# Performance work log

Measured on AMD Instinct MI355X. Metric: run time of the kernel, lower is better.

Reference implementation:

```python
import jax, jax.numpy as jnp
import numpy as np

N_NODES = 100000
IN_F = 256
OUT_F = 256
N_EDGES = 3200000


def setup_inputs() -> dict:
    key = jax.random.key(0)
    ks = jax.random.split(key, 10)
    return {
        "mean": jax.random.normal(ks[0], (N_NODES, IN_F), dtype=jnp.float32),
        "var": jax.random.uniform(ks[1], (N_NODES, IN_F), dtype=jnp.float32),
        "W_mean": jax.random.normal(ks[2], (IN_F, OUT_F), dtype=jnp.float32) * (1.0 / np.sqrt(IN_F)),
        "b_mean": jax.random.normal(ks[3], (OUT_F,), dtype=jnp.float32) * 0.01,
        "W_var": jax.random.normal(ks[4], (IN_F, OUT_F), dtype=jnp.float32) * (1.0 / np.sqrt(IN_F)),
        "b_var": jax.random.normal(ks[5], (OUT_F,), dtype=jnp.float32) * 0.01,
        "edge_row": jax.random.randint(ks[6], (N_EDGES,), 0, N_NODES, dtype=jnp.int32),
        "edge_col": jax.random.randint(ks[7], (N_EDGES,), 0, N_NODES, dtype=jnp.int32),
        "adj0_vals": jax.random.uniform(ks[8], (N_EDGES,), dtype=jnp.float32),
        "adj1_vals": jax.random.uniform(ks[9], (N_EDGES,), dtype=jnp.float32),
    }


def _spmm(row, col, vals, x, n_nodes):
    # out[i] = sum_{e: row[e]==i} vals[e] * x[col[e]]
    gathered = x[col] * vals[:, None]  # [E, F]
    return jax.ops.segment_sum(gathered, row, num_segments=n_nodes)


def reference(mean, var, W_mean, b_mean, W_var, b_var, edge_row, edge_col, adj0_vals, adj1_vals):
    m = jnp.dot(mean, W_mean) + b_mean          # mean_conv
    v = jnp.dot(var, W_var) + b_var             # var_conv (initial=False)
    m = jax.nn.elu(m)                           # act0
    v = jax.nn.relu(v)                          # act1
    attention = jnp.exp(-v)
    m = m * attention
    v = v * attention * attention
    m = _spmm(edge_row, edge_col, adj0_vals, m, mean.shape[0])
    v = _spmm(edge_row, edge_col, adj1_vals, v, mean.shape[0])
    return (m, v)
```

## Files before the change

kernel.cpp:

```cpp
#include <hip/hip_runtime.h>
#include <hip/hip_bf16.h>
#include <stdint.h>

#define F 256
#define KSTEP 32

typedef short bhalf8 __attribute__((ext_vector_type(8)));
typedef unsigned short ushort8v __attribute__((ext_vector_type(8)));
typedef float f32x4 __attribute__((ext_vector_type(4)));
typedef int i32x4 __attribute__((ext_vector_type(4)));

__device__ __forceinline__ unsigned short f2b(float f) {
    union { float f; uint32_t u; } x; x.f = f;
    uint32_t u = x.u;
    return (unsigned short)((u + 0x7FFFu + ((u >> 16) & 1u)) >> 16);
}
__device__ __forceinline__ float b2f(unsigned short h) {
    union { uint32_t u; float f; } x; x.u = ((uint32_t)h) << 16;
    return x.f;
}

__global__ __launch_bounds__(256) void setup_kernel(
    const float* __restrict__ Wm, const float* __restrict__ Wv,
    unsigned short* __restrict__ Wt, int* __restrict__ count, int N)
{
    if (blockIdx.x < 98) {
        int gi = blockIdx.x * 1024 + threadIdx.x * 4;
        #pragma unroll
        for (int q = 0; q < 4; ++q)
            if (gi + q < N) count[gi + q] = 0;
        return;
    }
    int idx = (blockIdx.x - 98) * 256 + threadIdx.x;
    int sel = idx >> 11;
    int ks  = (idx >> 8) & 7;
    int n   = idx & 255;
    const float* W = sel ? Wv : Wm;
    unsigned short* dst = Wt + ((size_t)sel * 8 * 256 * 32) + ((size_t)(ks * 256 + n) * 32);
    #pragma unroll
    for (int kk = 0; kk < 32; ++kk)
        dst[kk] = f2b(W[(ks * 32 + kk) * 256 + n]);
}

__global__ void hist_kernel(const int* __restrict__ row, int E, int* __restrict__ count) {
    int i = blockIdx.x * blockDim.x + threadIdx.x;
    if (i < E) atomicAdd(&count[row[i]], 1);
}

__global__ __launch_bounds__(256) void scan1_kernel(const int* __restrict__ count, int N,
                                                    int* __restrict__ offs, int* __restrict__ bsums)
{
    __shared__ int sd[256];
    int t  = threadIdx.x;
    int gi = blockIdx.x * 1024 + t * 4;
    int c[4];
    #pragma unroll
    for (int q = 0; q < 4; ++q) c[q] = (gi + q < N) ? count[gi + q] : 0;
    int s = c[0] + c[1] + c[2] + c[3];
    sd[t] = s; __syncthreads();
    int acc = s;
    for (int off = 1; off < 256; off <<= 1) {
        int u = (t >= off) ? sd[t - off] : 0;
        __syncthreads();
        acc += u; sd[t] = acc;
        __syncthreads();
    }
    int run = acc - s;
    #pragma unroll
    for (int q = 0; q < 4; ++q) { if (gi + q < N) offs[gi + q] = run; run += c[q]; }
    if (t == 255) bsums[blockIdx.x] = acc;
}

__global__ __launch_bounds__(128) void scan2_kernel(int* __restrict__ bsums, int SB,
                                                    int* __restrict__ offs, int N, int E)
{
    __shared__ int sd[128];
    int t = threadIdx.x;
    int v = (t < SB) ? bsums[t] : 0;
    sd[t] = v; __syncthreads();
    int acc = v;
    for (int off = 1; off < 128; off <<= 1) {
        int u = (t >= off) ? sd[t - off] : 0;
        __syncthreads();
        acc += u; sd[t] = acc;
        __syncthreads();
    }
    if (t < SB) bsums[t] = acc - v;
    if (t == 127) offs[N] = E;
}

__global__ __launch_bounds__(256) void scan3_kernel(int* __restrict__ offs, int N,
                                                    const int* __restrict__ bsums,
                                                    int* __restrict__ cursor)
{
    int b  = bsums[blockIdx.x];
    int gi = blockIdx.x * 1024 + threadIdx.x * 4;
    #pragma unroll
    for (int q = 0; q < 4; ++q)
        if (gi + q < N) {
            int v = offs[gi + q] + b;
            offs[gi + q]   = v;
            cursor[gi + q] = v;
        }
}

__global__ __launch_bounds__(512) void dense_fill_kernel(
    const float* __restrict__ mean, const float* __restrict__ var,
    const unsigned short* __restrict__ Wt,
    const float* __restrict__ bm, const float* __restrict__ bv,
    unsigned short* __restrict__ mv, int N, int DB,
    const int* __restrict__ erow, const int* __restrict__ ecol,
    const float* __restrict__ a0, const float* __restrict__ a1,
    int E, int* __restrict__ cursor, i32x4* __restrict__ rec)
{
    __shared__ unsigned short Asm[64][40];
    __shared__ unsigned short Asv[64][40];
    __shared__ unsigned short Bsm[256][40];
    __shared__ unsigned short Bsv[256][40];

    const int g = blockIdx.x / 5;
    const int r = blockIdx.x % 5;

    if (r != 4) {
        int fid = g * 4 + r;
        int i = fid * 512 + threadIdx.x;
        if (i < E) {
            int   rr = erow[i];
            int   c  = ecol[i];
            float v0 = a0[i];
            float v1 = a1[i];
            int pos = atomicAdd(&cursor[rr], 1);
            i32x4 rc;
            rc[0] = c;
            rc[1] = __float_as_int(v0);
            rc[2] = __float_as_int(v1);
            rc[3] = 0;
            rec[pos] = rc;
        }
        return;
    }

    const int dbid = g;
    if (dbid >= DB) return;
    const int tid  = threadIdx.x;
    const int row0 = dbid * 64;
    const int lane = tid & 63;
    const int w    = tid >> 6;
    const int wr   = w >> 2;
    const int wc   = w & 3;
    const int lr   = lane & 15;
    const int lk   = lane >> 4;

    f32x4 accm[2][4], accv[2][4];
    #pragma unroll
    for (int i = 0; i < 2; ++i)
        #pragma unroll
        for (int j = 0; j < 4; ++j) { accm[i][j] = (f32x4)0.f; accv[i][j] = (f32x4)0.f; }

    const int srow = tid >> 3;
    const int skq  = (tid & 7) * 4;
    int sgrow = row0 + srow; if (sgrow >= N) sgrow = N - 1;

    const unsigned short* WtV = Wt + (size_t)8 * 256 * 32;

    for (int ks = 0; ks < F / KSTEP; ++ks) {
        const int k0 = ks * KSTEP;
        {
            const float4 am = *(const float4*)&mean[(size_t)sgrow * F + k0 + skq];
            const float4 av = *(const float4*)&var [(size_t)sgrow * F + k0 + skq];
            ushort4 um = { f2b(am.x), f2b(am.y), f2b(am.z), f2b(am.w) };
            ushort4 uv = { f2b(av.x), f2b(av.y), f2b(av.z), f2b(av.w) };
            *(ushort4*)&Asm[srow][skq] = um;
            *(ushort4*)&Asv[srow][skq] = uv;
        }
        {
            const unsigned short* sm = Wt  + (size_t)(ks * 256) * 32;
            const unsigned short* sv = WtV + (size_t)(ks * 256) * 32;
            #pragma unroll
            for (int h = 0; h < 2; ++h) {
                int c = tid + h * 512;
                int n = c >> 2, q = c & 3;
                *(ushort8v*)&Bsm[n][q * 8] = *(const ushort8v*)(sm + (size_t)n * 32 + q * 8);
                *(ushort8v*)&Bsv[n][q * 8] = *(const ushort8v*)(sv + (size_t)n * 32 + q * 8);
            }
        }
        __syncthreads();

        bhalf8 am0 = *(const bhalf8*)&Asm[wr*32 +  0 + lr][lk*8];
        bhalf8 am1 = *(const bhalf8*)&Asm[wr*32 + 16 + lr][lk*8];
        bhalf8 av0 = *(const bhalf8*)&Asv[wr*32 +  0 + lr][lk*8];
        bhalf8 av1 = *(const bhalf8*)&Asv[wr*32 + 16 + lr][lk*8];
        #pragma unroll
        for (int ct = 0; ct < 4; ++ct) {
            bhalf8 bmf = *(const bhalf8*)&Bsm[wc*64 + ct*16 + lr][lk*8];
            bhalf8 bvf = *(const bhalf8*)&Bsv[wc*64 + ct*16 + lr][lk*8];
            accm[0][ct] = __builtin_amdgcn_mfma_f32_16x16x32_bf16(am0, bmf, accm[0][ct], 0, 0, 0);
            accm[1][ct] = __builtin_amdgcn_mfma_f32_16x16x32_bf16(am1, bmf, accm[1][ct], 0, 0, 0);
            accv[0][ct] = __builtin_amdgcn_mfma_f32_16x16x32_bf16(av0, bvf, accv[0][ct], 0, 0, 0);
            accv[1][ct] = __builtin_amdgcn_mfma_f32_16x16x32_bf16(av1, bvf, accv[1][ct], 0, 0, 0);
        }
        __syncthreads();
    }

    #pragma unroll
    for (int rt = 0; rt < 2; ++rt) {
        #pragma unroll
        for (int ct = 0; ct < 4; ++ct) {
            const int col = wc*64 + ct*16 + lr;
            const float bmc = bm[col], bvc = bv[col];
            #pragma unroll
            for (int q = 0; q < 4; ++q) {
                int grow = row0 + wr*32 + rt*16 + lk*4 + q;
                if (grow < N) {
                    float mp = accm[rt][ct][q] + bmc;
                    float vp = accv[rt][ct][q] + bvc;
                    float me = mp > 0.f ? mp : (__expf(mp) - 1.f);
                    float vr = vp > 0.f ? vp : 0.f;
                    float att = __expf(-vr);
                    mv[(size_t)grow * 512 + col]       = f2b(me * att);
                    mv[(size_t)grow * 512 + 256 + col] = f2b(vr * att * att);
                }
            }
        }
    }
}

__global__ __launch_bounds__(256) void spmm_kernel(
    const int* __restrict__ offs, const int* __restrict__ rec,
    const unsigned short* __restrict__ mv,
    float* __restrict__ out, int N)
{
    int w    = threadIdx.x >> 6;
    int lane = threadIdx.x & 63;
    int node = blockIdx.x * 4 + w;
    if (node >= N) return;
    int s = offs[node], e = offs[node + 1];

    const bool isv = lane >= 32;
    const int  fb  = (lane & 31) * 8;
    const unsigned short* base = mv + (isv ? 256 : 0) + fb;
    const int woff = isv ? 2 : 1;

    float acc[8];
    #pragma unroll
    for (int q = 0; q < 8; ++q) acc[q] = 0.f;

    const int cnt = e - s;
    const int nb  = cnt >> 3;
    const int* rp = rec + (size_t)s * 4;

    if (nb > 0) {
        int   c[8];
        float wt[8];
        #pragma unroll
        for (int q = 0; q < 8; ++q) {
            c[q]  = __builtin_nontemporal_load(rp + q * 4);
            wt[q] = __int_as_float(__builtin_nontemporal_load(rp + q * 4 + woff));
        }
        for (int b = 0; b < nb; ++b) {
            ushort8v p[8];
            #pragma unroll
            for (int q = 0; q < 8; ++q)
                p[q] = *(const ushort8v*)(base + (size_t)c[q] * 512);
            int   cn[8];
            float wn[8];
            if (b + 1 < nb) {
                const int* rn = rp + 32;
                #pragma unroll
                for (int q = 0; q < 8; ++q) {
                    cn[q] = __builtin_nontemporal_load(rn + q * 4);
                    wn[q] = __int_as_float(__builtin_nontemporal_load(rn + q * 4 + woff));
                }
            }
            #pragma unroll
            for (int q = 0; q < 8; ++q) {
                #pragma unroll
                for (int t = 0; t < 8; ++t) acc[t] += wt[q] * b2f(p[q][t]);
            }
            #pragma unroll
            for (int q = 0; q < 8; ++q) { c[q] = cn[q]; wt[q] = wn[q]; }
            rp += 32;
        }
    }
    for (int j = s + nb * 8; j < e; ++j) {
        const int* rj = rec + (size_t)j * 4;
        int   cc = rj[0];
        float a  = __int_as_float(rj[woff]);
        ushort8v p = *(const ushort8v*)(base + (size_t)cc * 512);
        #pragma unroll
        for (int t = 0; t < 8; ++t) acc[t] += a * b2f(p[t]);
    }

    float* obase = out + (isv ? (size_t)N * F : 0) + (size_t)node * F + fb;
    float4 o0 = { acc[0], acc[1], acc[2], acc[3] };
    float4 o1 = { acc[4], acc[5], acc[6], acc[7] };
    *(float4*)obase       = o0;
    *(float4*)(obase + 4) = o1;
}

extern "C" void kernel_launch(void* const* d_in, const int* in_sizes, int n_in,
                              void* d_out, int out_size, void* d_ws, size_t ws_size,
                              hipStream_t stream)
{
    const float* mean = (const float*)d_in[0];
    const float* var  = (const float*)d_in[1];
    const float* Wm   = (const float*)d_in[2];
    const float* bm   = (const float*)d_in[3];
    const float* Wv   = (const float*)d_in[4];
    const float* bv   = (const float*)d_in[5];
    const int*   erow = (const int*)d_in[6];
    const int*   ecol = (const int*)d_in[7];
    const float* a0   = (const float*)d_in[8];
    const float* a1   = (const float*)d_in[9];

    const int N = in_sizes[0] / F;
    const int E = in_sizes[6];

    uintptr_t p = (uintptr_t)d_ws;
    auto take = [&](size_t bytes) {
        uintptr_t r = (p + 255) & ~(uintptr_t)255;
        p = r + bytes;
        return (void*)r;
    };
    unsigned short* mv     = (unsigned short*)take((size_t)N * 512 * 2);
    int*            rec    = (int*)take((size_t)E * 16);
    int*            count  = (int*)take((size_t)N * 4);
    int*            offs   = (int*)take((size_t)(N + 1) * 4);
    int*            cursor = (int*)take((size_t)N * 4);
    int*            bsums  = (int*)take(1024 * 4);
    unsigned short* Wt     = (unsigned short*)take((size_t)2 * 8 * 256 * 32 * 2);

    const int SB = (N + 1023) / 1024;
    const int DB = (N + 63) / 64;
    const int FB = (E + 511) / 512;
    int groups = (DB > (FB + 3) / 4) ? DB : (FB + 3) / 4;
    int total  = groups * 5;

    setup_kernel<<<114, 256, 0, stream>>>(Wm, Wv, Wt, count, N);
    hist_kernel<<<(E + 255) / 256, 256, 0, stream>>>(erow, E, count);
    scan1_kernel<<<SB, 256, 0, stream>>>(count, N, offs, bsums);
    scan2_kernel<<<1, 128, 0, stream>>>(bsums, SB, offs, N, E);
    scan3_kernel<<<SB, 256, 0, stream>>>(offs, N, bsums, cursor);
    dense_fill_kernel<<<total, 512, 0, stream>>>(mean, var, Wt, bm, bv, mv, N, DB,
                                                 erow, ecol, a0, a1, E, cursor, (i32x4*)rec);
    spmm_kernel<<<(N + 3) / 4, 256, 0, stream>>>(offs, rec, mv, (float*)d_out, N);
}
```

Baseline: 798.1 us.

## Replace CSR histogram/scan build with fixed-capacity per-node edge buckets plus overflow

Edges are scattered directly into per-node slots of capacity 64 using atomic counters, eliminating the histogram and three scan kernels. Rows exceeding capacity go to a bounded overflow list handled by an atomic-add kernel after the SpMM. This needs a much larger workspace and falls back to the old CSR path if it is unavailable. Overflow beyond the fixed list cap would drop edges, so correctness depends on the degree distribution.

```diff
diff --git a/kernel.cpp b/kernel.cpp
--- a/kernel.cpp
+++ b/kernel.cpp
@@ -4,6 +4,8 @@
 
 #define F 256
 #define KSTEP 32
+#define CAP 64
+#define OVMAX 200000
 
 typedef short bhalf8 __attribute__((ext_vector_type(8)));
 typedef unsigned short ushort8v __attribute__((ext_vector_type(8)));
@@ -22,9 +24,11 @@
 
 __global__ __launch_bounds__(256) void setup_kernel(
     const float* __restrict__ Wm, const float* __restrict__ Wv,
-    unsigned short* __restrict__ Wt, int* __restrict__ count, int N)
+    unsigned short* __restrict__ Wt, int* __restrict__ count,
+    int* __restrict__ ovcnt, int N)
 {
     if (blockIdx.x < 98) {
+        if (blockIdx.x == 0 && threadIdx.x == 0 && ovcnt) *ovcnt = 0;
         int gi = blockIdx.x * 1024 + threadIdx.x * 4;
         #pragma unroll
         for (int q = 0; q < 4; ++q)
@@ -40,6 +44,246 @@
     #pragma unroll
     for (int kk = 0; kk < 32; ++kk)
         dst[kk] = f2b(W[(ks * 32 + kk) * 256 + n]);
+}
+
+__device__ __forceinline__ void dense_tile(
+    const float* __restrict__ mean, const float* __restrict__ var,
+    const unsigned short* __restrict__ Wt,
+    const float* __restrict__ bm, const float* __restrict__ bv,
+    unsigned short* __restrict__ mv, int N, int dbid,
+    unsigned short (*Asm)[40], unsigned short (*Asv)[40],
+    unsigned short (*Bsm)[40], unsigned short (*Bsv)[40])
+{
+    const int tid  = threadIdx.x;
+    const int row0 = dbid * 64;
+    const int lane = tid & 63;
+    const int w    = tid >> 6;
+    const int wr   = w >> 2;
+    const int wc   = w & 3;
+    const int lr   = lane & 15;
+    const int lk   = lane >> 4;
+
+    f32x4 accm[2][4], accv[2][4];
+    #pragma unroll
+    for (int i = 0; i < 2; ++i)
+        #pragma unroll
+        for (int j = 0; j < 4; ++j) { accm[i][j] = (f32x4)0.f; accv[i][j] = (f32x4)0.f; }
+
+    const int srow = tid >> 3;
+    const int skq  = (tid & 7) * 4;
+    int sgrow = row0 + srow; if (sgrow >= N) sgrow = N - 1;
+
+    const unsigned short* WtV = Wt + (size_t)8 * 256 * 32;
+
+    for (int ks = 0; ks < F / KSTEP; ++ks) {
+        const int k0 = ks * KSTEP;
+        {
+            const float4 am = *(const float4*)&mean[(size_t)sgrow * F + k0 + skq];
+            const float4 av = *(const float4*)&var [(size_t)sgrow * F + k0 + skq];
+            ushort4 um = { f2b(am.x), f2b(am.y), f2b(am.z), f2b(am.w) };
+            ushort4 uv = { f2b(av.x), f2b(av.y), f2b(av.z), f2b(av.w) };
+            *(ushort4*)&Asm[srow][skq] = um;
+            *(ushort4*)&Asv[srow][skq] = uv;
+        }
+        {
+            const unsigned short* sm = Wt  + (size_t)(ks * 256) * 32;
+            const unsigned short* sv = WtV + (size_t)(ks * 256) * 32;
+            #pragma unroll
+            for (int h = 0; h < 2; ++h) {
+                int c = tid + h * 512;
+                int n = c >> 2, q = c & 3;
+                *(ushort8v*)&Bsm[n][q * 8] = *(const ushort8v*)(sm + (size_t)n * 32 + q * 8);
+                *(ushort8v*)&Bsv[n][q * 8] = *(const ushort8v*)(sv + (size_t)n * 32 + q * 8);
+            }
+        }
+        __syncthreads();
+
+        bhalf8 am0 = *(const bhalf8*)&Asm[wr*32 +  0 + lr][lk*8];
+        bhalf8 am1 = *(const bhalf8*)&Asm[wr*32 + 16 + lr][lk*8];
+        bhalf8 av0 = *(const bhalf8*)&Asv[wr*32 +  0 + lr][lk*8];
+        bhalf8 av1 = *(const bhalf8*)&Asv[wr*32 + 16 + lr][lk*8];
+        #pragma unroll
+        for (int ct = 0; ct < 4; ++ct) {
+            bhalf8 bmf = *(const bhalf8*)&Bsm[wc*64 + ct*16 + lr][lk*8];
+            bhalf8 bvf = *(const bhalf8*)&Bsv[wc*64 + ct*16 + lr][lk*8];
+            accm[0][ct] = __builtin_amdgcn_mfma_f32_16x16x32_bf16(am0, bmf, accm[0][ct], 0, 0, 0);
+            accm[1][ct] = __builtin_amdgcn_mfma_f32_16x16x32_bf16(am1, bmf, accm[1][ct], 0, 0, 0);
+            accv[0][ct] = __builtin_amdgcn_mfma_f32_16x16x32_bf16(av0, bvf, accv[0][ct], 0, 0, 0);
+            accv[1][ct] = __builtin_amdgcn_mfma_f32_16x16x32_bf16(av1, bvf, accv[1][ct], 0, 0, 0);
+        }
+        __syncthreads();
+    }
+
+    #pragma unroll
+    for (int rt = 0; rt < 2; ++rt) {
+        #pragma unroll
+        for (int ct = 0; ct < 4; ++ct) {
+            const int col = wc*64 + ct*16 + lr;
+            const float bmc = bm[col], bvc = bv[col];
+            #pragma unroll
+            for (int q = 0; q < 4; ++q) {
+                int grow = row0 + wr*32 + rt*16 + lk*4 + q;
+                if (grow < N) {
+                    float mp = accm[rt][ct][q] + bmc;
+                    float vp = accv[rt][ct][q] + bvc;
+                    float me = mp > 0.f ? mp : (__expf(mp) - 1.f);
+                    float vr = vp > 0.f ? vp : 0.f;
+                    float att = __expf(-vr);
+                    mv[(size_t)grow * 512 + col]       = f2b(me * att);
+                    mv[(size_t)grow * 512 + 256 + col] = f2b(vr * att * att);
+                }
+            }
+        }
+    }
+}
+
+__global__ __launch_bounds__(512) void dense_fill_bucket_kernel(
+    const float* __restrict__ mean, const float* __restrict__ var,
+    const unsigned short* __restrict__ Wt,
+    const float* __restrict__ bm, const float* __restrict__ bv,
+    unsigned short* __restrict__ mv, int N, int DB,
+    const int* __restrict__ erow, const int* __restrict__ ecol,
+    const float* __restrict__ a0, const float* __restrict__ a1,
+    int E, int* __restrict__ count, i32x4* __restrict__ slots,
+    int* __restrict__ ovcnt, i32x4* __restrict__ ovlist)
+{
+    __shared__ unsigned short Asm[64][40];
+    __shared__ unsigned short Asv[64][40];
+    __shared__ unsigned short Bsm[256][40];
+    __shared__ unsigned short Bsv[256][40];
+
+    const int g = blockIdx.x / 5;
+    const int r = blockIdx.x % 5;
+
+    if (r != 4) {
+        int i = (g * 4 + r) * 512 + threadIdx.x;
+        if (i < E) {
+            int   rr = erow[i];
+            int   c  = ecol[i];
+            float v0 = a0[i];
+            float v1 = a1[i];
+            int pos = atomicAdd(&count[rr], 1);
+            if (pos < CAP) {
+                i32x4 rc;
+                rc[0] = c;
+                rc[1] = __float_as_int(v0);
+                rc[2] = __float_as_int(v1);
+                rc[3] = 0;
+                slots[(size_t)rr * CAP + pos] = rc;
+            } else {
+                int o = atomicAdd(ovcnt, 1);
+                if (o < OVMAX) {
+                    i32x4 rc;
+                    rc[0] = rr;
+                    rc[1] = c;
+                    rc[2] = __float_as_int(v0);
+                    rc[3] = __float_as_int(v1);
+                    ovlist[o] = rc;
+                }
+            }
+        }
+        return;
+    }
+    if (g >= DB) return;
+    dense_tile(mean, var, Wt, bm, bv, mv, N, g, Asm, Asv, Bsm, Bsv);
+}
+
+__global__ __launch_bounds__(256) void spmm_bucket_kernel(
+    const int* __restrict__ count, const int* __restrict__ slots,
+    const unsigned short* __restrict__ mv,
+    float* __restrict__ out, int N)
+{
+    int w    = threadIdx.x >> 6;
+    int lane = threadIdx.x & 63;
+    int node = blockIdx.x * 4 + w;
+    if (node >= N) return;
+    int cnt = count[node];
+    if (cnt > CAP) cnt = CAP;
+
+    const bool isv = lane >= 32;
+    const int  fb  = (lane & 31) * 8;
+    const unsigned short* base = mv + (isv ? 256 : 0) + fb;
+    const int woff = isv ? 2 : 1;
+
+    float acc[8];
+    #pragma unroll
+    for (int q = 0; q < 8; ++q) acc[q] = 0.f;
+
+    const int nb  = cnt >> 3;
+    const int* rp = slots + (size_t)node * CAP * 4;
+    const int* rp0 = rp;
+
+    if (nb > 0) {
+        int   c[8];
+        float wt[8];
+        #pragma unroll
+        for (int q = 0; q < 8; ++q) {
+            c[q]  = __builtin_nontemporal_load(rp + q * 4);
+            wt[q] = __int_as_float(__builtin_nontemporal_load(rp + q * 4 + woff));
+        }
+        for (int b = 0; b < nb; ++b) {
+            ushort8v p[8];
+            #pragma unroll
+            for (int q = 0; q < 8; ++q)
+                p[q] = *(const ushort8v*)(base + (size_t)c[q] * 512);
+            int   cn[8];
+            float wn[8];
+            if (b + 1 < nb) {
+                const int* rn = rp + 32;
+                #pragma unroll
+                for (int q = 0; q < 8; ++q) {
+                    cn[q] = __builtin_nontemporal_load(rn + q * 4);
+                    wn[q] = __int_as_float(__builtin_nontemporal_load(rn + q * 4 + woff));
+                }
+            }
+            #pragma unroll
+            for (int q = 0; q < 8; ++q) {
+                #pragma unroll
+                for (int t = 0; t < 8; ++t) acc[t] += wt[q] * b2f(p[q][t]);
+            }
+            #pragma unroll
+            for (int q = 0; q < 8; ++q) { c[q] = cn[q]; wt[q] = wn[q]; }
+            rp += 32;
+        }
+    }
+    for (int j = nb * 8; j < cnt; ++j) {
+        const int* rj = rp0 + (size_t)j * 4;
+        int   cc = rj[0];
+        float a  = __int_as_float(rj[woff]);
+        ushort8v p = *(const ushort8v*)(base + (size_t)cc * 512);
+        #pragma unroll
+        for (int t = 0; t < 8; ++t) acc[t] += a * b2f(p[t]);
+    }
+
+    float* obase = out + (isv ? (size_t)N * F : 0) + (size_t)node * F + fb;
+    float4 o0 = { acc[0], acc[1], acc[2], acc[3] };
+    float4 o1 = { acc[4], acc[5], acc[6], acc[7] };
+    *(float4*)obase       = o0;
+    *(float4*)(obase + 4) = o1;
+}
+
+__global__ __launch_bounds__(256) void overflow_kernel(
+    const int* __restrict__ ovcnt, const i32x4* __restrict__ ovlist,
+    const unsigned short* __restrict__ mv, float* __restrict__ out, int N)
+{
+    int nov = *ovcnt;
+    if (nov > OVMAX) nov = OVMAX;
+    if (nov == 0) return;
+    int gw   = (blockIdx.x * 256 + threadIdx.x) >> 6;
+    int nw   = (gridDim.x * 256) >> 6;
+    int lane = threadIdx.x & 63;
+    const bool isv = lane >= 32;
+    const int  fb  = (lane & 31) * 8;
+    for (int e = gw; e < nov; e += nw) {
+        i32x4 rc = ovlist[e];
+        int row = rc[0], c = rc[1];
+        float a = __int_as_float(isv ? rc[3] : rc[2]);
+        const unsigned short* p = mv + (size_t)c * 512 + (isv ? 256 : 0) + fb;
+        float* ob = out + (isv ? (size_t)N * F : 0) + (size_t)row * F + fb;
+        #pragma unroll
+        for (int t = 0; t < 8; ++t)
+            atomicAdd(&ob[t], a * b2f(p[t]));
+    }
 }
 
 __global__ void hist_kernel(const int* __restrict__ row, int E, int* __restrict__ count) {
@@ -122,8 +366,7 @@
     const int r = blockIdx.x % 5;
 
     if (r != 4) {
-        int fid = g * 4 + r;
-        int i = fid * 512 + threadIdx.x;
+        int i = (g * 4 + r) * 512 + threadIdx.x;
         if (i < E) {
             int   rr = erow[i];
             int   c  = ecol[i];
@@ -139,90 +382,8 @@
         }
         return;
     }
-
-    const int dbid = g;
-    if (dbid >= DB) return;
-    const int tid  = threadIdx.x;
-    const int row0 = dbid * 64;
-    const int lane = tid & 63;
-    const int w    = tid >> 6;
-    const int wr   = w >> 2;
-    const int wc   = w & 3;
-    const int lr   = lane & 15;
-    const int lk   = lane >> 4;
-
-    f32x4 accm[2][4], accv[2][4];
-    #pragma unroll
-    for (int i = 0; i < 2; ++i)
-        #pragma unroll
-        for (int j = 0; j < 4; ++j) { accm[i][j] = (f32x4)0.f; accv[i][j] = (f32x4)0.f; }
-
-    const int srow = tid >> 3;
-    const int skq  = (tid & 7) * 4;
-    int sgrow = row0 + srow; if (sgrow >= N) sgrow = N - 1;
-
-    const unsigned short* WtV = Wt + (size_t)8 * 256 * 32;
-
-    for (int ks = 0; ks < F / KSTEP; ++ks) {
-        const int k0 = ks * KSTEP;
-        {
-            const float4 am = *(const float4*)&mean[(size_t)sgrow * F + k0 + skq];
-            const float4 av = *(const float4*)&var [(size_t)sgrow * F + k0 + skq];
-            ushort4 um = { f2b(am.x), f2b(am.y), f2b(am.z), f2b(am.w) };
-            ushort4 uv = { f2b(av.x), f2b(av.y), f2b(av.z), f2b(av.w) };
-            *(ushort4*)&Asm[srow][skq] = um;
-            *(ushort4*)&Asv[srow][skq] = uv;
-        }
-        {
-            const unsigned short* sm = Wt  + (size_t)(ks * 256) * 32;
-            const unsigned short* sv = WtV + (size_t)(ks * 256) * 32;
-            #pragma unroll
-            for (int h = 0; h < 2; ++h) {
-                int c = tid + h * 512;
-                int n = c >> 2, q = c & 3;
-                *(ushort8v*)&Bsm[n][q * 8] = *(const ushort8v*)(sm + (size_t)n * 32 + q * 8);
-                *(ushort8v*)&Bsv[n][q * 8] = *(const ushort8v*)(sv + (size_t)n * 32 + q * 8);
-            }
-        }
-        __syncthreads();
-
-        bhalf8 am0 = *(const bhalf8*)&Asm[wr*32 +  0 + lr][lk*8];
-        bhalf8 am1 = *(const bhalf8*)&Asm[wr*32 + 16 + lr][lk*8];
-        bhalf8 av0 = *(const bhalf8*)&Asv[wr*32 +  0 + lr][lk*8];
-        bhalf8 av1 = *(const bhalf8*)&Asv[wr*32 + 16 + lr][lk*8];
-        #pragma unroll
-        for (int ct = 0; ct < 4; ++ct) {
-            bhalf8 bmf = *(const bhalf8*)&Bsm[wc*64 + ct*16 + lr][lk*8];
-            bhalf8 bvf = *(const bhalf8*)&Bsv[wc*64 + ct*16 + lr][lk*8];
-            accm[0][ct] = __builtin_amdgcn_mfma_f32_16x16x32_bf16(am0, bmf, accm[0][ct], 0, 0, 0);
-            accm[1][ct] = __builtin_amdgcn_mfma_f32_16x16x32_bf16(am1, bmf, accm[1][ct], 0, 0, 0);
-            accv[0][ct] = __builtin_amdgcn_mfma_f32_16x16x32_bf16(av0, bvf, accv[0][ct], 0, 0, 0);
-            accv[1][ct] = __builtin_amdgcn_mfma_f32_16x16x32_bf16(av1, bvf, accv[1][ct], 0, 0, 0);
-        }
-        __syncthreads();
-    }
-
-    #pragma unroll
-    for (int rt = 0; rt < 2; ++rt) {
-        #pragma unroll
-        for (int ct = 0; ct < 4; ++ct) {
-            const int col = wc*64 + ct*16 + lr;
-            const float bmc = bm[col], bvc = bv[col];
-            #pragma unroll
-            for (int q = 0; q < 4; ++q) {
-                int grow = row0 + wr*32 + rt*16 + lk*4 + q;
-                if (grow < N) {
-                    float mp = accm[rt][ct][q] + bmc;
-                    float vp = accv[rt][ct][q] + bvc;
-                    float me = mp > 0.f ? mp : (__expf(mp) - 1.f);
-                    float vr = vp > 0.f ? vp : 0.f;
-                    float att = __expf(-vr);
-                    mv[(size_t)grow * 512 + col]       = f2b(me * att);
-                    mv[(size_t)grow * 512 + 256 + col] = f2b(vr * att * att);
-                }
-            }
-        }
-    }
+    if (g >= DB) return;
+    dense_tile(mean, var, Wt, bm, bv, mv, N, g, Asm, Asv, Bsm, Bsv);
 }
 
 __global__ __launch_bounds__(256) void spmm_kernel(
@@ -316,32 +477,64 @@
     const int N = in_sizes[0] / F;
     const int E = in_sizes[6];
 
+    const int DB = (N + 63) / 64;
+    const int FB = (E + 511) / 512;
+    int groups = (DB > (FB + 3) / 4) ? DB : (FB + 3) / 4;
+    int total  = groups * 5;
+
     uintptr_t p = (uintptr_t)d_ws;
     auto take = [&](size_t bytes) {
         uintptr_t r = (p + 255) & ~(uintptr_t)255;
         p = r + bytes;
         return (void*)r;
     };
-    unsigned short* mv     = (unsigned short*)take((size_t)N * 512 * 2);
-    int*            rec    = (int*)take((size_t)E * 16);
-    int*            count  = (int*)take((size_t)N * 4);
-    int*            offs   = (int*)take((size_t)(N + 1) * 4);
-    int*            cursor = (int*)take((size_t)N * 4);
-    int*            bsums  = (int*)take(1024 * 4);
-    unsigned short* Wt     = (unsigned short*)take((size_t)2 * 8 * 256 * 32 * 2);
-
-    const int SB = (N + 1023) / 1024;
-    const int DB = (N + 63) / 64;
-    const int FB = (E + 511) / 512;
-    int groups = (DB > (FB + 3) / 4) ? DB : (FB + 3) / 4;
-    int total  = groups * 5;
-
-    setup_kernel<<<114, 256, 0, stream>>>(Wm, Wv, Wt, count, N);
-    hist_kernel<<<(E + 255) / 256, 256, 0, stream>>>(erow, E, count);
-    scan1_kernel<<<SB, 256, 0, stream>>>(count, N, offs, bsums);
-    scan2_kernel<<<1, 128, 0, stream>>>(bsums, SB, offs, N, E);
-    scan3_kernel<<<SB, 256, 0, stream>>>(offs, N, bsums, cursor);
-    dense_fill_kernel<<<total, 512, 0, stream>>>(mean, var, Wt, bm, bv, mv, N, DB,
-                                                 erow, ecol, a0, a1, E, cursor, (i32x4*)rec);
-    spmm_kernel<<<(N + 3) / 4, 256, 0, stream>>>(offs, rec, mv, (float*)d_out, N);
-}
+
+    size_t need = 0;
+    {
+        size_t q = 0;
+        auto sim = [&](size_t b) { q = ((q + 255) & ~(size_t)255) + b; };
+        sim((size_t)N * 512 * 2);
+        sim((size_t)N * CAP * 16);
+        sim((size_t)N * 4);
+        sim(256);
+        sim((size_t)OVMAX * 16);
+        sim((size_t)2 * 8 * 256 * 32 * 2);
+        need = q;
+    }
+
+    if (ws_size >= need) {
+        unsigned short* mv     = (unsigned short*)take((size_t)N * 512 * 2);
+        i32x4*          slots  = (i32x4*)take((size_t)N * CAP * 16);
+        int*            count  = (int*)take((size_t)N * 4);
+        int*            ovcnt  = (int*)take(256);
+        i32x4*          ovlist = (i32x4*)take((size_t)OVMAX * 16);
+        unsigned short* Wt     = (unsigned short*)take((size_t)2 * 8 * 256 * 32 * 2);
+
+        setup_kernel<<<114, 256, 0, stream>>>(Wm, Wv, Wt, count, ovcnt, N);
+        dense_fill_bucket_kernel<<<total, 512, 0, stream>>>(
+            mean, var, Wt, bm, bv, mv, N, DB,
+            erow, ecol, a0, a1, E, count, slots, ovcnt, ovlist);
+        spmm_bucket_kernel<<<(N + 3) / 4, 256, 0, stream>>>(
+            count, (const int*)slots, mv, (float*)d_out, N);
+        overflow_kernel<<<16, 256, 0, stream>>>(ovcnt, ovlist, mv, (float*)d_out, N);
+    } else {
+        unsigned short* mv     = (unsigned short*)take((size_t)N * 512 * 2);
+        int*            rec    = (int*)take((size_t)E * 16);
+        int*            count  = (int*)take((size_t)N * 4);
+        int*            offs   = (int*)take((size_t)(N + 1) * 4);
+        int*            cursor = (int*)take((size_t)N * 4);
+        int*            bsums  = (int*)take(1024 * 4);
+        unsigned short* Wt     = (unsigned short*)take((size_t)2 * 8 * 256 * 32 * 2);
+
+        const int SB = (N + 1023) / 1024;
+
+        setup_kernel<<<114, 256, 0, stream>>>(Wm, Wv, Wt, count, (int*)nullptr, N);
+        hist_kernel<<<(E + 255) / 256, 256, 0, stream>>>(erow, E, count);
+        scan1_kernel<<<SB, 256, 0, stream>>>(count, N, offs, bsums);
+        scan2_kernel<<<1, 128, 0, stream>>>(bsums, SB, offs, N, E);
+        scan3_kernel<<<SB, 256, 0, stream>>>(offs, N, bsums, cursor);
+        dense_fill_kernel<<<total, 512, 0, stream>>>(mean, var, Wt, bm, bv, mv, N, DB,
+                                                     erow, ecol, a0, a1, E, cursor, (i32x4*)rec);
+        spmm_kernel<<<(N + 3) / 4, 256, 0, stream>>>(offs, rec, mv, (float*)d_out, N);
+    }
+}
```

After: 657.2 us. 1.21x faster.

## Replace CSR build with fixed-capacity per-row buckets plus overflow list

Applied to the files above, without the earlier changes.

Removes the histogram and three-stage prefix-scan kernels by scattering edges directly into fixed 64-slot buckets per row, using the atomic count as the slot index. Records shrink to 8 bytes by packing both edge weights as bf16. Rows with more than 64 edges spill to an overflow list that a separate kernel handles with float atomics. This trades memory footprint and weight precision for fewer launches and less index traffic, and the overflow list caps at 200000 entries.

```diff
diff --git a/kernel.cpp b/kernel.cpp
--- a/kernel.cpp
+++ b/kernel.cpp
@@ -4,11 +4,14 @@
 
 #define F 256
 #define KSTEP 32
+#define CAP 64
+#define OVMAX 200000
 
 typedef short bhalf8 __attribute__((ext_vector_type(8)));
 typedef unsigned short ushort8v __attribute__((ext_vector_type(8)));
 typedef float f32x4 __attribute__((ext_vector_type(4)));
 typedef int i32x4 __attribute__((ext_vector_type(4)));
+typedef unsigned int u32x2 __attribute__((ext_vector_type(2)));
 
 __device__ __forceinline__ unsigned short f2b(float f) {
     union { float f; uint32_t u; } x; x.f = f;
@@ -22,9 +25,11 @@
 
 __global__ __launch_bounds__(256) void setup_kernel(
     const float* __restrict__ Wm, const float* __restrict__ Wv,
-    unsigned short* __restrict__ Wt, int* __restrict__ count, int N)
+    unsigned short* __restrict__ Wt, int* __restrict__ count,
+    int* __restrict__ ovcnt, int N)
 {
     if (blockIdx.x < 98) {
+        if (blockIdx.x == 0 && threadIdx.x == 0) *ovcnt = 0;
         int gi = blockIdx.x * 1024 + threadIdx.x * 4;
         #pragma unroll
         for (int q = 0; q < 4; ++q)
@@ -42,106 +47,14 @@
         dst[kk] = f2b(W[(ks * 32 + kk) * 256 + n]);
 }
 
-__global__ void hist_kernel(const int* __restrict__ row, int E, int* __restrict__ count) {
-    int i = blockIdx.x * blockDim.x + threadIdx.x;
-    if (i < E) atomicAdd(&count[row[i]], 1);
-}
-
-__global__ __launch_bounds__(256) void scan1_kernel(const int* __restrict__ count, int N,
-                                                    int* __restrict__ offs, int* __restrict__ bsums)
-{
-    __shared__ int sd[256];
-    int t  = threadIdx.x;
-    int gi = blockIdx.x * 1024 + t * 4;
-    int c[4];
-    #pragma unroll
-    for (int q = 0; q < 4; ++q) c[q] = (gi + q < N) ? count[gi + q] : 0;
-    int s = c[0] + c[1] + c[2] + c[3];
-    sd[t] = s; __syncthreads();
-    int acc = s;
-    for (int off = 1; off < 256; off <<= 1) {
-        int u = (t >= off) ? sd[t - off] : 0;
-        __syncthreads();
-        acc += u; sd[t] = acc;
-        __syncthreads();
-    }
-    int run = acc - s;
-    #pragma unroll
-    for (int q = 0; q < 4; ++q) { if (gi + q < N) offs[gi + q] = run; run += c[q]; }
-    if (t == 255) bsums[blockIdx.x] = acc;
-}
-
-__global__ __launch_bounds__(128) void scan2_kernel(int* __restrict__ bsums, int SB,
-                                                    int* __restrict__ offs, int N, int E)
-{
-    __shared__ int sd[128];
-    int t = threadIdx.x;
-    int v = (t < SB) ? bsums[t] : 0;
-    sd[t] = v; __syncthreads();
-    int acc = v;
-    for (int off = 1; off < 128; off <<= 1) {
-        int u = (t >= off) ? sd[t - off] : 0;
-        __syncthreads();
-        acc += u; sd[t] = acc;
-        __syncthreads();
-    }
-    if (t < SB) bsums[t] = acc - v;
-    if (t == 127) offs[N] = E;
-}
-
-__global__ __launch_bounds__(256) void scan3_kernel(int* __restrict__ offs, int N,
-                                                    const int* __restrict__ bsums,
-                                                    int* __restrict__ cursor)
-{
-    int b  = bsums[blockIdx.x];
-    int gi = blockIdx.x * 1024 + threadIdx.x * 4;
-    #pragma unroll
-    for (int q = 0; q < 4; ++q)
-        if (gi + q < N) {
-            int v = offs[gi + q] + b;
-            offs[gi + q]   = v;
-            cursor[gi + q] = v;
-        }
-}
-
-__global__ __launch_bounds__(512) void dense_fill_kernel(
+__device__ __forceinline__ void dense_tile(
     const float* __restrict__ mean, const float* __restrict__ var,
     const unsigned short* __restrict__ Wt,
     const float* __restrict__ bm, const float* __restrict__ bv,
-    unsigned short* __restrict__ mv, int N, int DB,
-    const int* __restrict__ erow, const int* __restrict__ ecol,
-    const float* __restrict__ a0, const float* __restrict__ a1,
-    int E, int* __restrict__ cursor, i32x4* __restrict__ rec)
-{
-    __shared__ unsigned short Asm[64][40];
-    __shared__ unsigned short Asv[64][40];
-    __shared__ unsigned short Bsm[256][40];
-    __shared__ unsigned short Bsv[256][40];
-
-    const int g = blockIdx.x / 5;
-    const int r = blockIdx.x % 5;
-
-    if (r != 4) {
-        int fid = g * 4 + r;
-        int i = fid * 512 + threadIdx.x;
-        if (i < E) {
-            int   rr = erow[i];
-            int   c  = ecol[i];
-            float v0 = a0[i];
-            float v1 = a1[i];
-            int pos = atomicAdd(&cursor[rr], 1);
-            i32x4 rc;
-            rc[0] = c;
-            rc[1] = __float_as_int(v0);
-            rc[2] = __float_as_int(v1);
-            rc[3] = 0;
-            rec[pos] = rc;
-        }
-        return;
-    }
-
-    const int dbid = g;
-    if (dbid >= DB) return;
+    unsigned short* __restrict__ mv, int N, int dbid,
+    unsigned short (*Asm)[40], unsigned short (*Asv)[40],
+    unsigned short (*Bsm)[40], unsigned short (*Bsv)[40])
+{
     const int tid  = threadIdx.x;
     const int row0 = dbid * 64;
     const int lane = tid & 63;
@@ -225,8 +138,57 @@
     }
 }
 
-__global__ __launch_bounds__(256) void spmm_kernel(
-    const int* __restrict__ offs, const int* __restrict__ rec,
+__global__ __launch_bounds__(512) void dense_fill_bucket_kernel(
+    const float* __restrict__ mean, const float* __restrict__ var,
+    const unsigned short* __restrict__ Wt,
+    const float* __restrict__ bm, const float* __restrict__ bv,
+    unsigned short* __restrict__ mv, int N, int DB,
+    const int* __restrict__ erow, const int* __restrict__ ecol,
+    const float* __restrict__ a0, const float* __restrict__ a1,
+    int E, int* __restrict__ count, u32x2* __restrict__ slots,
+    int* __restrict__ ovcnt, i32x4* __restrict__ ovlist)
+{
+    __shared__ unsigned short Asm[64][40];
+    __shared__ unsigned short Asv[64][40];
+    __shared__ unsigned short Bsm[256][40];
+    __shared__ unsigned short Bsv[256][40];
+
+    const int g = blockIdx.x / 5;
+    const int r = blockIdx.x % 5;
+
+    if (r != 4) {
+        int i = (g * 4 + r) * 512 + threadIdx.x;
+        if (i < E) {
+            int   rr = erow[i];
+            int   c  = ecol[i];
+            float v0 = a0[i];
+            float v1 = a1[i];
+            int pos = atomicAdd(&count[rr], 1);
+            if (pos < CAP) {
+                u32x2 rc;
+                rc[0] = (unsigned)c;
+                rc[1] = (unsigned)f2b(v0) | ((unsigned)f2b(v1) << 16);
+                slots[(size_t)rr * CAP + pos] = rc;
+            } else {
+                int o = atomicAdd(ovcnt, 1);
+                if (o < OVMAX) {
+                    i32x4 rc;
+                    rc[0] = rr;
+                    rc[1] = c;
+                    rc[2] = __float_as_int(v0);
+                    rc[3] = __float_as_int(v1);
+                    ovlist[o] = rc;
+                }
+            }
+        }
+        return;
+    }
+    if (g >= DB) return;
+    dense_tile(mean, var, Wt, bm, bv, mv, N, g, Asm, Asv, Bsm, Bsv);
+}
+
+__global__ __launch_bounds__(256) void spmm_bucket_kernel(
+    const int* __restrict__ count, const u32x2* __restrict__ slots,
     const unsigned short* __restrict__ mv,
     float* __restrict__ out, int N)
 {
@@ -234,28 +196,30 @@
     int lane = threadIdx.x & 63;
     int node = blockIdx.x * 4 + w;
     if (node >= N) return;
-    int s = offs[node], e = offs[node + 1];
+    int cnt = count[node];
+    if (cnt > CAP) cnt = CAP;
 
     const bool isv = lane >= 32;
     const int  fb  = (lane & 31) * 8;
     const unsigned short* base = mv + (isv ? 256 : 0) + fb;
-    const int woff = isv ? 2 : 1;
+    const int sh = isv ? 16 : 0;
 
     float acc[8];
     #pragma unroll
     for (int q = 0; q < 8; ++q) acc[q] = 0.f;
 
-    const int cnt = e - s;
     const int nb  = cnt >> 3;
-    const int* rp = rec + (size_t)s * 4;
+    const u32x2* rp  = slots + (size_t)node * CAP;
+    const u32x2* rp0 = rp;
 
     if (nb > 0) {
         int   c[8];
         float wt[8];
         #pragma unroll
         for (int q = 0; q < 8; ++q) {
-            c[q]  = __builtin_nontemporal_load(rp + q * 4);
-            wt[q] = __int_as_float(__builtin_nontemporal_load(rp + q * 4 + woff));
+            u32x2 rc = __builtin_nontemporal_load(rp + q);
+            c[q]  = (int)rc[0];
+            wt[q] = b2f((unsigned short)(rc[1] >> sh));
         }
         for (int b = 0; b < nb; ++b) {
             ushort8v p[8];
@@ -265,11 +229,12 @@
             int   cn[8];
             float wn[8];
             if (b + 1 < nb) {
-                const int* rn = rp + 32;
+                const u32x2* rn = rp + 8;
                 #pragma unroll
                 for (int q = 0; q < 8; ++q) {
-                    cn[q] = __builtin_nontemporal_load(rn + q * 4);
-                    wn[q] = __int_as_float(__builtin_nontemporal_load(rn + q * 4 + woff));
+                    u32x2 rc = __builtin_nontemporal_load(rn + q);
+                    cn[q] = (int)rc[0];
+                    wn[q] = b2f((unsigned short)(rc[1] >> sh));
                 }
             }
             #pragma unroll
@@ -279,13 +244,13 @@
             }
             #pragma unroll
             for (int q = 0; q < 8; ++q) { c[q] = cn[q]; wt[q] = wn[q]; }
-            rp += 32;
-        }
-    }
-    for (int j = s + nb * 8; j < e; ++j) {
-        const int* rj = rec + (size_t)j * 4;
-        int   cc = rj[0];
-        float a  = __int_as_float(rj[woff]);
+            rp += 8;
+        }
+    }
+    for (int j = nb * 8; j < cnt; ++j) {
+        u32x2 rc = rp0[j];
+        int   cc = (int)rc[0];
+        float a  = b2f((unsigned short)(rc[1] >> sh));
         ushort8v p = *(const ushort8v*)(base + (size_t)cc * 512);
         #pragma unroll
         for (int t = 0; t < 8; ++t) acc[t] += a * b2f(p[t]);
@@ -296,6 +261,30 @@
     float4 o1 = { acc[4], acc[5], acc[6], acc[7] };
     *(float4*)obase       = o0;
     *(float4*)(obase + 4) = o1;
+}
+
+__global__ __launch_bounds__(256) void overflow_kernel(
+    const int* __restrict__ ovcnt, const i32x4* __restrict__ ovlist,
+    const unsigned short* __restrict__ mv, float* __restrict__ out, int N)
+{
+    int nov = *ovcnt;
+    if (nov > OVMAX) nov = OVMAX;
+    if (nov == 0) return;
+    int gw   = (blockIdx.x * 256 + threadIdx.x) >> 6;
+    int nw   = (gridDim.x * 256) >> 6;
+    int lane = threadIdx.x & 63;
+    const bool isv = lane >= 32;
+    const int  fb  = (lane & 31) * 8;
+    for (int e = gw; e < nov; e += nw) {
+        i32x4 rc = ovlist[e];
+        int row = rc[0], c = rc[1];
+        float a = __int_as_float(isv ? rc[3] : rc[2]);
+        const unsigned short* p = mv + (size_t)c * 512 + (isv ? 256 : 0) + fb;
+        float* ob = out + (isv ? (size_t)N * F : 0) + (size_t)row * F + fb;
+        #pragma unroll
+        for (int t = 0; t < 8; ++t)
+            atomicAdd(&ob[t], a * b2f(p[t]));
+    }
 }
 
 extern "C" void kernel_launch(void* const* d_in, const int* in_sizes, int n_in,
@@ -316,32 +305,30 @@
     const int N = in_sizes[0] / F;
     const int E = in_sizes[6];
 
+    const int DB = (N + 63) / 64;
+    const int FB = (E + 511) / 512;
+    int groups = (DB > (FB + 3) / 4) ? DB : (FB + 3) / 4;
+    int total  = groups * 5;
+
     uintptr_t p = (uintptr_t)d_ws;
     auto take = [&](size_t bytes) {
         uintptr_t r = (p + 255) & ~(uintptr_t)255;
         p = r + bytes;
         return (void*)r;
     };
+
     unsigned short* mv     = (unsigned short*)take((size_t)N * 512 * 2);
-    int*            rec    = (int*)take((size_t)E * 16);
+    u32x2*          slots  = (u32x2*)take((size_t)N * CAP * 8);
     int*            count  = (int*)take((size_t)N * 4);
-    int*            offs   = (int*)take((size_t)(N + 1) * 4);
-    int*            cursor = (int*)take((size_t)N * 4);
-    int*            bsums  = (int*)take(1024 * 4);
+    int*            ovcnt  = (int*)take(256);
+    i32x4*          ovlist = (i32x4*)take((size_t)OVMAX * 16);
     unsigned short* Wt     = (unsigned short*)take((size_t)2 * 8 * 256 * 32 * 2);
 
-    const int SB = (N + 1023) / 1024;
-    const int DB = (N + 63) / 64;
-    const int FB = (E + 511) / 512;
-    int groups = (DB > (FB + 3) / 4) ? DB : (FB + 3) / 4;
-    int total  = groups * 5;
-
-    setup_kernel<<<114, 256, 0, stream>>>(Wm, Wv, Wt, count, N);
-    hist_kernel<<<(E + 255) / 256, 256, 0, stream>>>(erow, E, count);
-    scan1_kernel<<<SB, 256, 0, stream>>>(count, N, offs, bsums);
-    scan2_kernel<<<1, 128, 0, stream>>>(bsums, SB, offs, N, E);
-    scan3_kernel<<<SB, 256, 0, stream>>>(offs, N, bsums, cursor);
-    dense_fill_kernel<<<total, 512, 0, stream>>>(mean, var, Wt, bm, bv, mv, N, DB,
-                                                 erow, ecol, a0, a1, E, cursor, (i32x4*)rec);
-    spmm_kernel<<<(N + 3) / 4, 256, 0, stream>>>(offs, rec, mv, (float*)d_out, N);
-}
+    setup_kernel<<<114, 256, 0, stream>>>(Wm, Wv, Wt, count, ovcnt, N);
+    dense_fill_bucket_kernel<<<total, 512, 0, stream>>>(
+        mean, var, Wt, bm, bv, mv, N, DB,
+        erow, ecol, a0, a1, E, count, slots, ovcnt, ovlist);
+    spmm_bucket_kernel<<<(N + 3) / 4, 256, 0, stream>>>(
+        count, slots, mv, (float*)d_out, N);
+    overflow_kernel<<<16, 256, 0, stream>>>(ovcnt, ovlist, mv, (float*)d_out, N);
+}
```

Result: faster. 678.6 us (-15.0%).
